# Kernel tuning notes

Hardware: AMD Instinct MI355X
Metric: run time of the kernel (lower is better)

## Reference

```python
import jax, jax.numpy as jnp
import numpy as np

INDEX_SHIFT = jnp.array([[0, 0], [-1, 0], [1, 0], [0, 1], [-1, 1], [1, 1], [0, -1], [-1, -1], [1, -1]], dtype=jnp.int32)
GRID = jnp.array([513, 513], dtype=jnp.int32)  # pseudo_image_dims + 1


def setup_inputs() -> dict:
    key = jax.random.key(0)
    k1, k2, k3, k4 = jax.random.split(key, 4)
    li_bev_coors = jax.random.randint(k1, (8192, 2), 0, 512, dtype=jnp.int32)
    ra_bev_coors = jax.random.randint(k2, (2048, 2), 0, 512, dtype=jnp.int32)
    ra_pts = jax.random.normal(k3, (2048, 5), dtype=jnp.float32)
    ra_voxel_coords = jax.random.randint(k4, (2048, 3), 0, 512, dtype=jnp.int32)
    return {"li_bev_coors": li_bev_coors, "ra_bev_coors": ra_bev_coors,
            "ra_pts": ra_pts, "ra_voxel_coords": ra_voxel_coords}


def _neighbour_coors(bev_grids):
    # [N,2] -> [N,9,2]: shift by 9-neighborhood, wrap by (grid_size+1)
    return (bev_grids[:, None, :] + INDEX_SHIFT[None, :, :]) % GRID


def _nearest_dy(neighbour_coor, dy_coor, dy_mask):
    # neighbour_coor: [N,9,2] int; dy_coor: [M,2] float; dy_mask: [M] bool
    n = neighbour_coor.shape[0]
    a = neighbour_coor.reshape(-1, 2).astype(jnp.float32)        # [N*9, 2]
    a2 = jnp.sum(a * a, axis=-1)                                  # [N*9]
    b2 = jnp.sum(dy_coor * dy_coor, axis=-1)                      # [M]
    # squared euclidean distances (exact: integer coordinates)
    d2 = a2[:, None] + b2[None, :] - 2.0 * (a @ dy_coor.T)        # [N*9, M]
    d2 = jnp.where(dy_mask[None, :], d2, jnp.inf)                 # mask non-dynamic voxels
    dmin = jnp.sqrt(jnp.maximum(jnp.min(d2, axis=-1), 0.0))       # min commutes with sqrt
    return (dmin * 0.01).reshape(n, 9)


def reference(li_bev_coors, ra_bev_coors, ra_pts, ra_voxel_coords):
    # dynamic-point selection: |velocity| > 0.1 (column 4)
    dy_mask = jnp.abs(ra_pts[:, 4]) > 0.1                         # [M]
    dy_coor = ra_voxel_coords[:, 1:].astype(jnp.float32)          # [M,2]
    # (uniquifying dy_coor does not change the min-distance; skip for jit shapes)
    li_nb = _neighbour_coors(li_bev_coors)                        # [N_li,9,2]
    ra_nb = _neighbour_coors(ra_bev_coors)                        # [N_ra,9,2]
    use = jnp.sum(dy_mask) > 1
    li_dis = jnp.where(use, _nearest_dy(li_nb, dy_coor, dy_mask), 0.0)
    ra_dis = jnp.where(use, _nearest_dy(ra_nb, dy_coor, dy_mask), 0.0)
    return (li_dis, ra_dis)
```

## Files before the change

### kernel.cpp

```cpp
#include <hip/hip_runtime.h>

#define NW    16
#define BLOCK (NW * 64)
#define QPT   6
#define QPB   (64 * QPT)
#define MAXM  2048


typedef float v2f __attribute__((ext_vector_type(2)));

__device__ __forceinline__ v2f pkfma(v2f a, v2f b, v2f c) {
    return __builtin_elementwise_fma(a, b, c);
}

__global__ __launch_bounds__(BLOCK) void gauss_kernel(
    const int* __restrict__ li_coors, int n_li,
    const int* __restrict__ ra_coors, int n_ra,
    const float* __restrict__ pts,
    const int* __restrict__ vox,
    int m,
    float* __restrict__ out, int total)
{
    __shared__ __align__(16) float sx[MAXM];
    __shared__ __align__(16) float sy[MAXM];
    __shared__ __align__(16) float part[NW * QPB];
    __shared__ float q2s[QPB];
    __shared__ int s_cnt;

    const int tid  = threadIdx.x;
    const int lane = tid & 63;
    const int w    = tid >> 6;

    if (tid == 0) s_cnt = 0;

    const int qbase = blockIdx.x * QPB;
    const int li_total = n_li * 9;
    float nx[QPT], ny[QPT], q2[QPT], mn[QPT];
#pragma unroll
    for (int k = 0; k < QPT; ++k) {
        int q = qbase + lane + 64 * k;
        float qx = 0.0f, qy = 0.0f;
        if (q < total) {
            const int shift_x[9] = {0,-1,1,0,-1,1,0,-1,1};
            const int shift_y[9] = {0, 0,0,1, 1,1,-1,-1,-1};
            int n, s;
            const int* src;
            if (q < li_total) { n = q / 9; s = q - n * 9; src = li_coors; }
            else { int r = q - li_total; n = r / 9; s = r - n * 9; src = ra_coors; }
            int cx = src[n * 2 + 0] + shift_x[s];
            int cy = src[n * 2 + 1] + shift_y[s];
            if (cx < 0) cx += 513;
            if (cy < 0) cy += 513;
            qx = (float)cx; qy = (float)cy;
        }
        nx[k] = -2.0f * qx;
        ny[k] = -2.0f * qy;
        q2[k] = fmaf(qx, qx, qy * qy);
        mn[k] = 3.4e38f;
    }

    for (int base = 0; base < m; base += MAXM) {
        const int cs  = min(m - base, MAXM);
        int per = (cs + NW - 1) / NW;
        per = (per + 3) & ~3;
        const int tot = NW * per;

        __syncthreads();
        for (int i = tid; i < tot; i += BLOCK) {
            int gi = base + i;
            float x = 3.0e4f, y = 3.0e4f;
            bool dyn = false;
            if (i < cs && fabsf(pts[gi * 5 + 4]) > 0.1f) {
                dyn = true;
                x = (float)vox[gi * 3 + 1];
                y = (float)vox[gi * 3 + 2];
            }
            sx[i] = x;
            sy[i] = y;
            unsigned long long b = __ballot(dyn);
            if (lane == 0 && b) atomicAdd(&s_cnt, (int)__popcll(b));
        }
        __syncthreads();

        const float4* __restrict__ X4 = (const float4*)sx + ((w * per) >> 2);
        const float4* __restrict__ Y4 = (const float4*)sy + ((w * per) >> 2);
        const int iters = per >> 2;
#pragma unroll 4
        for (int i = 0; i < iters; ++i) {
            float4 X = X4[i];
            float4 Y = Y4[i];
            v2f X01 = {X.x, X.y}, X23 = {X.z, X.w};
            v2f Y01 = {Y.x, Y.y}, Y23 = {Y.z, Y.w};
            v2f C01 = pkfma(X01, X01, Y01 * Y01);
            v2f C23 = pkfma(X23, X23, Y23 * Y23);
#pragma unroll
            for (int k = 0; k < QPT; ++k) {
                v2f nx2 = {nx[k], nx[k]};
                v2f ny2 = {ny[k], ny[k]};
                v2f T01 = pkfma(X01, nx2, pkfma(Y01, ny2, C01));
                v2f T23 = pkfma(X23, nx2, pkfma(Y23, ny2, C23));
                mn[k] = fminf(fminf(T01.x, T01.y), mn[k]);
                mn[k] = fminf(fminf(T23.x, T23.y), mn[k]);
            }
        }
    }

#pragma unroll
    for (int k = 0; k < QPT; ++k)
        part[w * QPB + lane + 64 * k] = mn[k];
    if (w == 0) {
#pragma unroll
        for (int k = 0; k < QPT; ++k)
            q2s[lane + 64 * k] = q2[k];
    }
    __syncthreads();

    if (tid < QPB) {
        float v = 3.4e38f;
#pragma unroll
        for (int w2 = 0; w2 < NW; ++w2)
            v = fminf(v, part[w2 * QPB + tid]);
        int gq = qbase + tid;
        if (gq < total)
            out[gq] = (s_cnt > 1) ? sqrtf(fmaxf(q2s[tid] + v, 0.0f)) * 0.01f
                                  : 0.0f;
    }
}

extern "C" void kernel_launch(void* const* d_in, const int* in_sizes, int n_in,
                              void* d_out, int out_size, void* d_ws, size_t ws_size,
                              hipStream_t stream) {
    const int*   li  = (const int*)d_in[0];
    const int*   ra  = (const int*)d_in[1];
    const float* pts = (const float*)d_in[2];
    const int*   vox = (const int*)d_in[3];

    const int n_li = in_sizes[0] / 2;
    const int n_ra = in_sizes[1] / 2;
    const int m    = in_sizes[2] / 5;

    const int total  = (n_li + n_ra) * 9;
    const int blocks = (total + QPB - 1) / QPB;

    gauss_kernel<<<blocks, BLOCK, 0, stream>>>(
        li, n_li, ra, n_ra, pts, vox, m, (float*)d_out, total);
}
```

Baseline: 73.74 us.

## Hold candidate points in registers and broadcast queries via readlane

Reorganizes the nearest-distance loop so each lane keeps a slice of the 2048 candidate points (x, y and precomputed squared norm) in registers. Each wave then loops over 32 queries broadcast with readlane, instead of each lane streaming candidates from LDS for its own six queries. Block size drops from 1024 to 256 threads with 128 queries per block, and the reduction becomes a per-wave LDS transpose. This removes repeated LDS reads and per-candidate norm recomputation, at the cost of heavy register use (48 packed vectors plus 32 minima) and more blocks, each reloading the full candidate set.

```diff
diff --git a/kernel.cpp b/kernel.cpp
--- a/kernel.cpp
+++ b/kernel.cpp
@@ -1,10 +1,12 @@
 #include <hip/hip_runtime.h>
 
-#define NW    16
-#define BLOCK (NW * 64)
-#define QPT   6
-#define QPB   (64 * QPT)
-#define MAXM  2048
+#define BLOCK 256
+#define NWAVE 4
+#define WQ    32
+#define QPB   (NWAVE * WQ)
+#define CHUNK 2048
+#define NQUAD (CHUNK / 256)
+#define ROWP  68
 
 
 typedef float v2f __attribute__((ext_vector_type(2)));
@@ -12,8 +14,11 @@
 __device__ __forceinline__ v2f pkfma(v2f a, v2f b, v2f c) {
     return __builtin_elementwise_fma(a, b, c);
 }
+__device__ __forceinline__ float rdlane(float v, int l) {
+    return __int_as_float(__builtin_amdgcn_readlane(__float_as_int(v), l));
+}
 
-__global__ __launch_bounds__(BLOCK) void gauss_kernel(
+__global__ __launch_bounds__(BLOCK, 3) void gauss_kernel(
     const int* __restrict__ li_coors, int n_li,
     const int* __restrict__ ra_coors, int n_ra,
     const float* __restrict__ pts,
@@ -21,11 +26,12 @@
     int m,
     float* __restrict__ out, int total)
 {
-    __shared__ __align__(16) float sx[MAXM];
-    __shared__ __align__(16) float sy[MAXM];
-    __shared__ __align__(16) float part[NW * QPB];
-    __shared__ float q2s[QPB];
+    __shared__ __align__(16) float smem[NWAVE * WQ * ROWP];
     __shared__ int s_cnt;
+
+    float* __restrict__ SX = smem;
+    float* __restrict__ SY = smem + CHUNK;
+    float* __restrict__ SC = smem + 2 * CHUNK;
 
     const int tid  = threadIdx.x;
     const int lane = tid & 63;
@@ -33,14 +39,12 @@
 
     if (tid == 0) s_cnt = 0;
 
-    const int qbase = blockIdx.x * QPB;
+    const int qbase = blockIdx.x * QPB + w * WQ;
     const int li_total = n_li * 9;
-    float nx[QPT], ny[QPT], q2[QPT], mn[QPT];
-#pragma unroll
-    for (int k = 0; k < QPT; ++k) {
-        int q = qbase + lane + 64 * k;
-        float qx = 0.0f, qy = 0.0f;
-        if (q < total) {
+    float nx = 0.0f, ny = 0.0f, q2 = 0.0f;
+    {
+        int q = qbase + (lane & (WQ - 1));
+        if (lane < WQ && q < total) {
             const int shift_x[9] = {0,-1,1,0,-1,1,0,-1,1};
             const int shift_y[9] = {0, 0,0,1, 1,1,-1,-1,-1};
             int n, s;
@@ -51,22 +55,24 @@
             int cy = src[n * 2 + 1] + shift_y[s];
             if (cx < 0) cx += 513;
             if (cy < 0) cy += 513;
-            qx = (float)cx; qy = (float)cy;
+            float qx = (float)cx, qy = (float)cy;
+            nx = -2.0f * qx;
+            ny = -2.0f * qy;
+            q2 = fmaf(qx, qx, qy * qy);
         }
-        nx[k] = -2.0f * qx;
-        ny[k] = -2.0f * qy;
-        q2[k] = fmaf(qx, qx, qy * qy);
-        mn[k] = 3.4e38f;
     }
 
-    for (int base = 0; base < m; base += MAXM) {
-        const int cs  = min(m - base, MAXM);
-        int per = (cs + NW - 1) / NW;
-        per = (per + 3) & ~3;
-        const int tot = NW * per;
+    float mnq[WQ];
+#pragma unroll
+    for (int i = 0; i < WQ; ++i) mnq[i] = 3.4e38f;
+
+    v2f cx01[NQUAD], cx23[NQUAD], cy01[NQUAD], cy23[NQUAD], cc01[NQUAD], cc23[NQUAD];
+
+    for (int base = 0; base < m; base += CHUNK) {
+        const int cs = min(m - base, CHUNK);
 
         __syncthreads();
-        for (int i = tid; i < tot; i += BLOCK) {
+        for (int i = tid; i < CHUNK; i += BLOCK) {
             int gi = base + i;
             float x = 3.0e4f, y = 3.0e4f;
             bool dyn = false;
@@ -75,55 +81,64 @@
                 x = (float)vox[gi * 3 + 1];
                 y = (float)vox[gi * 3 + 2];
             }
-            sx[i] = x;
-            sy[i] = y;
+            SX[i] = x;
+            SY[i] = y;
+            SC[i] = fmaf(x, x, y * y);
             unsigned long long b = __ballot(dyn);
             if (lane == 0 && b) atomicAdd(&s_cnt, (int)__popcll(b));
         }
         __syncthreads();
 
-        const float4* __restrict__ X4 = (const float4*)sx + ((w * per) >> 2);
-        const float4* __restrict__ Y4 = (const float4*)sy + ((w * per) >> 2);
-        const int iters = per >> 2;
-#pragma unroll 4
-        for (int i = 0; i < iters; ++i) {
-            float4 X = X4[i];
-            float4 Y = Y4[i];
-            v2f X01 = {X.x, X.y}, X23 = {X.z, X.w};
-            v2f Y01 = {Y.x, Y.y}, Y23 = {Y.z, Y.w};
-            v2f C01 = pkfma(X01, X01, Y01 * Y01);
-            v2f C23 = pkfma(X23, X23, Y23 * Y23);
+        const float4* __restrict__ X4 = (const float4*)SX;
+        const float4* __restrict__ Y4 = (const float4*)SY;
+        const float4* __restrict__ C4 = (const float4*)SC;
 #pragma unroll
-            for (int k = 0; k < QPT; ++k) {
-                v2f nx2 = {nx[k], nx[k]};
-                v2f ny2 = {ny[k], ny[k]};
-                v2f T01 = pkfma(X01, nx2, pkfma(Y01, ny2, C01));
-                v2f T23 = pkfma(X23, nx2, pkfma(Y23, ny2, C23));
-                mn[k] = fminf(fminf(T01.x, T01.y), mn[k]);
-                mn[k] = fminf(fminf(T23.x, T23.y), mn[k]);
+        for (int j = 0; j < NQUAD; ++j) {
+            float4 X = X4[lane + 64 * j];
+            float4 Y = Y4[lane + 64 * j];
+            float4 C = C4[lane + 64 * j];
+            cx01[j] = v2f{X.x, X.y}; cx23[j] = v2f{X.z, X.w};
+            cy01[j] = v2f{Y.x, Y.y}; cy23[j] = v2f{Y.z, Y.w};
+            cc01[j] = v2f{C.x, C.y}; cc23[j] = v2f{C.z, C.w};
+        }
+
+#pragma unroll
+        for (int q = 0; q < WQ; ++q) {
+            float snx = rdlane(nx, q);
+            float sny = rdlane(ny, q);
+            v2f vnx = {snx, snx};
+            v2f vny = {sny, sny};
+            float mv = mnq[q];
+#pragma unroll
+            for (int j = 0; j < NQUAD; ++j) {
+                v2f T0 = pkfma(cx01[j], vnx, pkfma(cy01[j], vny, cc01[j]));
+                v2f T1 = pkfma(cx23[j], vnx, pkfma(cy23[j], vny, cc23[j]));
+                mv = fminf(fminf(T0.x, T0.y), mv);
+                mv = fminf(fminf(T1.x, T1.y), mv);
             }
+            mnq[q] = mv;
         }
     }
 
-#pragma unroll
-    for (int k = 0; k < QPT; ++k)
-        part[w * QPB + lane + 64 * k] = mn[k];
-    if (w == 0) {
-#pragma unroll
-        for (int k = 0; k < QPT; ++k)
-            q2s[lane + 64 * k] = q2[k];
-    }
     __syncthreads();
 
-    if (tid < QPB) {
+    float* __restrict__ wscr = smem + w * (WQ * ROWP);
+#pragma unroll
+    for (int q = 0; q < WQ; ++q)
+        wscr[q * ROWP + lane] = mnq[q];
+
+    if (lane < WQ) {
+        const float4* __restrict__ r4 = (const float4*)(wscr + lane * ROWP);
         float v = 3.4e38f;
 #pragma unroll
-        for (int w2 = 0; w2 < NW; ++w2)
-            v = fminf(v, part[w2 * QPB + tid]);
-        int gq = qbase + tid;
+        for (int j = 0; j < 16; ++j) {
+            float4 t = r4[j];
+            v = fminf(fminf(t.x, t.y), v);
+            v = fminf(fminf(t.z, t.w), v);
+        }
+        int gq = qbase + lane;
         if (gq < total)
-            out[gq] = (s_cnt > 1) ? sqrtf(fmaxf(q2s[tid] + v, 0.0f)) * 0.01f
-                                  : 0.0f;
+            out[gq] = (s_cnt > 1) ? sqrtf(fmaxf(q2 + v, 0.0f)) * 0.01f : 0.0f;
     }
 }
 
```

Result: slower. 75.98 us (+3.0%).
